# Performance work log

Measured on AMD Instinct MI355X. Metric: run time of the kernel, lower is better.

The kernel has to match this reference:

```python
import jax, jax.numpy as jnp
import numpy as np

H, W = 192, 256
NEAR, FAR = 0.1, 100.0
ALPHA_MAX = 0.99


def setup_inputs() -> dict:
    key = jax.random.key(0)
    k0, k1, k2, k3, k4 = jax.random.split(key, 5)
    N = 512
    # place cloud in front of camera (identity view matrix looks down +z here)
    positions = jax.random.normal(k0, (N, 3), dtype=jnp.float32) + jnp.array([0.0, 0.0, 4.0], jnp.float32)
    scales = jax.random.uniform(k1, (N, 3), dtype=jnp.float32) * 0.2 + 0.02
    rotations = jax.random.normal(k2, (N, 4), dtype=jnp.float32)
    opacities = jax.random.normal(k3, (N, 1), dtype=jnp.float32)
    colors = jax.random.uniform(k4, (N, 3), dtype=jnp.float32)
    view_matrix = jnp.eye(4, dtype=jnp.float32)
    background = jnp.ones(3, dtype=jnp.float32)
    return dict(positions=positions, scales=scales, rotations=rotations,
                opacities=opacities, colors=colors, view_matrix=view_matrix,
                background=background, fov_x=60)


def _quat_to_rot(q):
    q = q / jnp.linalg.norm(q, axis=-1, keepdims=True)
    w, x, y, z = q[:, 0], q[:, 1], q[:, 2], q[:, 3]
    R = jnp.stack([
        1 - 2 * (y * y + z * z), 2 * (x * y - w * z), 2 * (x * z + w * y),
        2 * (x * y + w * z), 1 - 2 * (x * x + z * z), 2 * (y * z - w * x),
        2 * (x * z - w * y), 2 * (y * z + w * x), 1 - 2 * (x * x + y * y)
    ], axis=-1).reshape(-1, 3, 3)
    return R


def reference(positions, scales, rotations, opacities, colors, view_matrix, background, fov_x):
    # --- 3D covariance: R diag(s^2) R^T ---
    R = _quat_to_rot(rotations)                               # (N,3,3)
    cov3d = jnp.einsum('nij,nj,nkj->nik', R, scales ** 2, R)  # (N,3,3)

    # --- projection to screen space ---
    fx = W / (2.0 * np.tan(np.deg2rad(float(fov_x)) / 2.0))
    Wr = view_matrix[:3, :3]
    t = view_matrix[:3, 3]
    cam = positions @ Wr.T + t[None, :]                       # (N,3)
    depths = cam[:, 2]
    zs = jnp.maximum(depths, NEAR)
    X, Y = cam[:, 0], cam[:, 1]
    mx = fx * X / zs + W / 2.0
    my = H / 2.0 - fx * Y / zs
    zero = jnp.zeros_like(zs)
    # Jacobian of perspective projection (N,2,3)
    J = jnp.stack([
        jnp.stack([fx / zs, zero, -fx * X / zs ** 2], axis=-1),
        jnp.stack([zero, fx / zs, -fx * Y / zs ** 2], axis=-1),
    ], axis=1)
    T = jnp.einsum('nij,jk->nik', J, Wr)                      # (N,2,3)
    cov2d = jnp.einsum('nij,njk,nlk->nil', T, cov3d, T)       # (N,2,2)
    cov2d = 0.5 * (cov2d + jnp.swapaxes(cov2d, 1, 2))

    a, b, c = cov2d[:, 0, 0], cov2d[:, 0, 1], cov2d[:, 1, 1]
    mean_e = 0.5 * (a + c)
    disc = jnp.sqrt(jnp.maximum(0.25 * (a - c) ** 2 + b ** 2, 0.0))
    min_eig = mean_e - disc
    eps = jnp.where(min_eig <= 0, jnp.abs(min_eig) + 1e-6, 0.0)
    a = a + eps
    c = c + eps
    max_eig = mean_e + eps + disc
    radii = jnp.ceil(3.0 * jnp.sqrt(jnp.maximum(max_eig, 1e-6)))

    # --- visibility + back-to-front (descending depth) order ---
    visible = (depths > NEAR) & (depths < FAR) & (radii > 0)
    order = jnp.argsort(jnp.where(visible, -depths, jnp.inf))
    a_s, b_s, c_s = a[order], b[order], c[order]
    mx_s, my_s = mx[order], my[order]
    op_s = jax.nn.sigmoid(opacities[order, 0])
    col_s = colors[order]
    vis_s = visible[order].astype(jnp.float32)

    # conic (inverse of 2x2 covariance)
    det = jnp.maximum(a_s * c_s - b_s * b_s, 1e-12)
    ca, cb, cc = c_s / det, -b_s / det, a_s / det

    xs = jnp.arange(W, dtype=jnp.float32)
    ys = jnp.arange(H, dtype=jnp.float32)
    dx = xs[None, None, :] - mx_s[:, None, None]              # (N,H,W)
    dy = ys[None, :, None] - my_s[:, None, None]              # (N,H,W)
    q = (ca[:, None, None] * dx * dx + 2.0 * cb[:, None, None] * dx * dy
         + cc[:, None, None] * dy * dy)
    G = jnp.exp(-0.5 * jnp.maximum(q, 0.0))                   # (N,H,W)
    alpha = jnp.clip(op_s[:, None, None] * G, 0.0, ALPHA_MAX) * vis_s[:, None, None]

    # exclusive cumulative transmittance T_i = prod_{j<i} (1 - alpha_j)
    Tc = jnp.cumprod(1.0 - alpha, axis=0)                     # (N,H,W)
    T_excl = jnp.concatenate([jnp.ones((1, H, W), alpha.dtype), Tc[:-1]], axis=0)
    image = jnp.einsum('nhw,nc->hwc', alpha * T_excl, col_s)  # (H,W,3)
    image = image + Tc[-1][..., None] * background[None, None, :]
    return image


if __name__ == '__main__':
    out = reference(**setup_inputs())
    print(out.shape, out.dtype)
```

## Files before the change

### kernel.cpp

```cpp
#include <hip/hip_runtime.h>
#include <math.h>

#define NG    512
#define IMG_W 256
#define IMG_H 192

#define NEAR_P    0.1f
#define FAR_P     100.0f
#define ALPHA_MAX 0.99f

#define PIX     64
#define CHUNKS  4
#define TPB     256

#define CULL_K  4.0f


__global__ __launch_bounds__(TPB) void gs_fused(
    const float* __restrict__ pos,
    const float* __restrict__ scl,
    const float* __restrict__ rot,
    const float* __restrict__ opa,
    const float* __restrict__ col,
    const float* __restrict__ vm,
    const int*   __restrict__ fov,
    const float* __restrict__ bg,
    float* __restrict__ out)
{
    __shared__ float4 s_cr0[NG];
    __shared__ float4 s_rec1[NG];
    __shared__ float  s_bcol[NG];
    __shared__ __align__(16) unsigned long long s_ku[NG + 2];
    __shared__ unsigned short s_list[NG];
    __shared__ int    s_wtot[4], s_woff[4], s_M, s_Mf;
    __shared__ float4 s_part[CHUNKS][PIX];
    __shared__ float  s_out[PIX*3];

    const int tid  = threadIdx.x;
    const int lane = tid & 63;
    const int wv   = tid >> 6;
    const int b    = blockIdx.x;
    const float yf  = (float)(b >> 2);
    const float x0f = (float)((b & 3) * PIX);

    const float fx = (float)IMG_W /
        (2.0f * __tanf((float)fov[0] * (float)(M_PI / 180.0) * 0.5f));

    const float W00 = vm[0],  W01 = vm[1],  W02 = vm[2],  t0 = vm[3];
    const float W10 = vm[4],  W11 = vm[5],  W12 = vm[6],  t1 = vm[7];
    const float W20 = vm[8],  W21 = vm[9],  W22 = vm[10], t2 = vm[11];

    #pragma unroll
    for (int gg = 0; gg < 2; ++gg) {
        const int g = tid + gg * TPB;
        float px = pos[g*3+0], py = pos[g*3+1], pz = pos[g*3+2];
        float X = W00*px + W01*py + W02*pz + t0;
        float Y = W10*px + W11*py + W12*pz + t1;
        float Z = W20*px + W21*py + W22*pz + t2;

        float zs = fmaxf(Z, NEAR_P);
        float rz = __fdividef(1.0f, zs);
        float fxrz = fx * rz;

        float mx = fxrz * X + (float)IMG_W * 0.5f;
        float my = (float)IMG_H * 0.5f - fxrz * Y;

        float s0 = scl[g*3+0], s1 = scl[g*3+1], s2 = scl[g*3+2];
        float smax2 = fmaxf(fmaxf(s0*s0, s1*s1), s2*s2);
        float Xr = X * rz, Yr = Y * rz;
        float J2 = fxrz*fxrz * (1.0f + Xr*Xr + Yr*Yr);
        float rb = CULL_K * sqrtf(smax2 * J2 + 1e-5f);

        bool visible = (Z > NEAR_P) && (Z < FAR_P);
        s_cr0[g] = make_float4(mx,
                               visible ? my : 1e30f,
                               visible ? rb : 0.0f,
                               visible ? -Z : INFINITY);
    }
    __syncthreads();

    const int g0 = 2*tid, g1 = g0 + 1;
    float4 cr0 = s_cr0[g0];
    float4 cr1 = s_cr0[g1];
    bool p0 = (fabsf(cr0.y - yf) <= cr0.z) &
              (cr0.x >= x0f - cr0.z) & (cr0.x <= x0f + 63.0f + cr0.z);
    bool p1 = (fabsf(cr1.y - yf) <= cr1.z) &
              (cr1.x >= x0f - cr1.z) & (cr1.x <= x0f + 63.0f + cr1.z);

    unsigned long long m0 = __ballot(p0);
    unsigned long long m1 = __ballot(p1);
    unsigned long long lt = (1ull << lane) - 1ull;

    if (lane == 0) s_wtot[wv] = __popcll(m0) + __popcll(m1);
    __syncthreads();
    if (tid == 0) {
        int acc = 0;
        for (int i = 0; i < 4; ++i) { s_woff[i] = acc; acc += s_wtot[i]; }
        s_M = acc;
        s_Mf = 0;
        s_ku[acc]     = ~0ull;
        s_ku[acc + 1] = ~0ull;
    }
    __syncthreads();
    int basep = s_woff[wv] + __popcll(m0 & lt) + __popcll(m1 & lt);
    if (p0) {
        unsigned u = __float_as_uint(cr0.w);
        unsigned mm = (u & 0x80000000u) ? ~u : (u | 0x80000000u);
        s_list[basep] = (unsigned short)g0;
        s_ku[basep] = (((unsigned long long)mm) << 16) | (unsigned)g0;
    }
    if (p1) {
        int p = basep + (p0 ? 1 : 0);
        unsigned u = __float_as_uint(cr1.w);
        unsigned mm = (u & 0x80000000u) ? ~u : (u | 0x80000000u);
        s_list[p] = (unsigned short)g1;
        s_ku[p] = (((unsigned long long)mm) << 16) | (unsigned)g1;
    }
    __syncthreads();

    const int M = s_M;

    bool   qpA[2]   = {false, false};
    float4 rec0A[2], rec1A[2];
    float  bcolA[2] = {0.0f, 0.0f};
    unsigned long long ktA[2] = {0, 0};

    #pragma unroll
    for (int half = 0; half < 2; ++half) {
        if (half == 1 && M <= TPB) continue;
        const int t = half * TPB + tid;
        bool qp = false;
        if (t < M) {
            const int g = s_list[t];
            ktA[half] = s_ku[t];

            float4 q4 = ((const float4*)rot)[g];
            float qw = q4.x, qx = q4.y, qy = q4.z, qz = q4.w;
            float rn = __frsqrt_rn(qw*qw + qx*qx + qy*qy + qz*qz);
            qw *= rn; qx *= rn; qy *= rn; qz *= rn;
            float R00 = 1.f - 2.f*(qy*qy + qz*qz);
            float R01 = 2.f*(qx*qy - qw*qz);
            float R02 = 2.f*(qx*qz + qw*qy);
            float R10 = 2.f*(qx*qy + qw*qz);
            float R11 = 1.f - 2.f*(qx*qx + qz*qz);
            float R12 = 2.f*(qy*qz - qw*qx);
            float R20 = 2.f*(qx*qz - qw*qy);
            float R21 = 2.f*(qy*qz + qw*qx);
            float R22 = 1.f - 2.f*(qx*qx + qy*qy);

            float s0 = scl[g*3+0], s1 = scl[g*3+1], s2 = scl[g*3+2];
            float q0 = s0*s0, q1 = s1*s1, q2 = s2*s2;
            float C00 = R00*R00*q0 + R01*R01*q1 + R02*R02*q2;
            float C01 = R00*R10*q0 + R01*R11*q1 + R02*R12*q2;
            float C02 = R00*R20*q0 + R01*R21*q1 + R02*R22*q2;
            float C11 = R10*R10*q0 + R11*R11*q1 + R12*R12*q2;
            float C12 = R10*R20*q0 + R11*R21*q1 + R12*R22*q2;
            float C22 = R20*R20*q0 + R21*R21*q1 + R22*R22*q2;

            float px = pos[g*3+0], py = pos[g*3+1], pz = pos[g*3+2];
            float X = W00*px + W01*py + W02*pz + t0;
            float Y = W10*px + W11*py + W12*pz + t1;
            float Z = W20*px + W21*py + W22*pz + t2;

            float zs = fmaxf(Z, NEAR_P);
            float rz = __fdividef(1.0f, zs);
            float fxrz = fx * rz;

            float mx = fxrz * X + (float)IMG_W * 0.5f;
            float my = (float)IMG_H * 0.5f - fxrz * Y;

            float j02 = -fxrz * X * rz;
            float j12 = -fxrz * Y * rz;
            float T00 = fxrz*W00 + j02*W20;
            float T01 = fxrz*W01 + j02*W21;
            float T02 = fxrz*W02 + j02*W22;
            float T10 = fxrz*W10 + j12*W20;
            float T11 = fxrz*W11 + j12*W21;
            float T12 = fxrz*W12 + j12*W22;

            float u0 = C00*T00 + C01*T01 + C02*T02;
            float u1 = C01*T00 + C11*T01 + C12*T02;
            float u2 = C02*T00 + C12*T01 + C22*T02;
            float v0 = C00*T10 + C01*T11 + C02*T12;
            float v1 = C01*T10 + C11*T11 + C12*T12;
            float v2 = C02*T10 + C12*T11 + C22*T12;
            float a    = T00*u0 + T01*u1 + T02*u2;
            float bcov = 0.5f * ((T00*v0 + T01*v1 + T02*v2) + (T10*u0 + T11*u1 + T12*u2));
            float c    = T10*v0 + T11*v1 + T12*v2;

            float mean_e = 0.5f * (a + c);
            float disc = sqrtf(fmaxf(0.25f*(a - c)*(a - c) + bcov*bcov, 0.0f));
            float min_eig = mean_e - disc;
            float eps = (min_eig <= 0.0f) ? (fabsf(min_eig) + 1e-6f) : 0.0f;
            a += eps; c += eps;

            float det  = fmaxf(a*c - bcov*bcov, 1e-12f);
            float rdet = __fdividef(1.0f, det);
            float ca = c * rdet, cbv = -bcov * rdet, cc = a * rdet;
            float op = __fdividef(1.0f, 1.0f + __expf(-opa[g]));

            float ex = CULL_K * sqrtf(fmaxf(a, 0.0f));
            float ey = CULL_K * sqrtf(fmaxf(c, 0.0f));
            qp = (fabsf(my - yf) <= ey) &
                 (mx >= x0f - ex) & (mx <= x0f + 63.0f + ex);

            rec0A[half] = make_float4(-0.5f*ca, -cbv, -0.5f*cc, mx);
            rec1A[half] = make_float4(my, op, col[g*3+0], col[g*3+1]);
            bcolA[half] = col[g*3+2];

            if (!qp) s_ku[t] = ~0ull;
        }
        unsigned long long mq = __ballot(qp);
        if (lane == 0) atomicAdd(&s_Mf, __popcll(mq));
        qpA[half] = qp;
    }
    __syncthreads();

    #pragma unroll
    for (int half = 0; half < 2; ++half) {
        if (half == 1 && M <= TPB) continue;
        const int t = half * TPB + tid;
        if (t < M && qpA[half]) {
            const unsigned long long kt = ktA[half];
            const ulonglong2* ku2 = (const ulonglong2*)s_ku;
            int r = 0;
            const int M2 = (M + 1) >> 1;
            for (int j = 0; j < M2; ++j) {
                ulonglong2 kv = ku2[j];
                r += (int)(kv.x < kt);
                r += (int)(kv.y < kt);
            }
            s_cr0[r]  = rec0A[half];
            s_rec1[r] = rec1A[half];
            s_bcol[r] = bcolA[half];
        }
    }
    __syncthreads();

    const int Mf = s_Mf;
    const int qn = (Mf + CHUNKS - 1) / CHUNKS;
    const int lpix  = tid & 63;
    const int chunk = tid >> 6;
    int start = chunk * qn; if (start > Mf) start = Mf;
    int end   = start + qn; if (end > Mf) end = Mf;

    const float fxp = x0f + (float)lpix;

    float Tr = 1.0f, ar = 0.0f, ag = 0.0f, abv = 0.0f;
    for (int i = start; i < end; ++i) {
        float4 r0 = s_cr0[i];
        float4 r1 = s_rec1[i];
        float  bc = s_bcol[i];
        float dx = fxp - r0.w;
        float dy = yf  - r1.x;
        float qv = (r0.x*dx)*dx + (r0.y*dx)*dy + (r0.z*dy)*dy;
        float G = __expf(fminf(qv, 0.0f));
        float alpha = fminf(r1.y * G, ALPHA_MAX);
        float wgt = alpha * Tr;
        ar  += wgt * r1.z;
        ag  += wgt * r1.w;
        abv += wgt * bc;
        Tr  *= (1.0f - alpha);
    }
    s_part[chunk][lpix] = make_float4(ar, ag, abv, Tr);
    __syncthreads();

    if (chunk == 0) {
        float4 c0 = s_part[0][lpix], c1 = s_part[1][lpix];
        float4 c2 = s_part[2][lpix], c3 = s_part[3][lpix];
        float T0 = c0.w, T01 = T0*c1.w, T012 = T01*c2.w, Tall = T012*c3.w;
        float r  = c0.x + T0*c1.x + T01*c2.x + T012*c3.x;
        float gc = c0.y + T0*c1.y + T01*c2.y + T012*c3.y;
        float bb = c0.z + T0*c1.z + T01*c2.z + T012*c3.z;
        s_out[3*lpix+0] = r  + Tall * bg[0];
        s_out[3*lpix+1] = gc + Tall * bg[1];
        s_out[3*lpix+2] = bb + Tall * bg[2];
    }
    __syncthreads();
    if (tid < PIX*3)
        out[b * (PIX*3) + tid] = s_out[tid];
}

extern "C" void kernel_launch(void* const* d_in, const int* in_sizes, int n_in,
                              void* d_out, int out_size, void* d_ws, size_t ws_size,
                              hipStream_t stream) {
    const float* pos = (const float*)d_in[0];
    const float* scl = (const float*)d_in[1];
    const float* rot = (const float*)d_in[2];
    const float* opa = (const float*)d_in[3];
    const float* col = (const float*)d_in[4];
    const float* vm  = (const float*)d_in[5];
    const float* bgp = (const float*)d_in[6];
    const int*   fov = (const int*)d_in[7];

    float* out = (float*)d_out;

    gs_fused<<<(IMG_H * IMG_W) / PIX, TPB, 0, stream>>>(
        pos, scl, rot, opa, col, vm, fov, bgp, out);
}
```

Before: 14.83 us.

## Stage inputs in LDS, fuse culling pass, use 32-bit sort keys

Positions and scales are loaded once per block into shared memory with coalesced float4 loads, and both the cull pass and the per-Gaussian setup read them from there. The coarse cull predicate and depth key are now computed in registers, which removes a shared-memory round trip and a barrier. The rank sort compares 32-bit depth keys, four per LDS read, with an index tie-break in place of the 64-bit key that packed the index. A union lets the staged input buffers share space with the later record and partial-sum arrays to save LDS, and it also drops a redundant clamp before sqrt. The risk is that depth ties now resolve by compacted-list position rather than Gaussian index, and that the union reuse depends on the barriers placed between its phases.

```diff
diff --git a/kernel.cpp b/kernel.cpp
--- a/kernel.cpp
+++ b/kernel.cpp
@@ -15,6 +15,11 @@
 
 #define CULL_K  4.0f
 
+
+union SB {
+    struct { float pos[NG*3]; float scl[NG*3]; } st;
+    struct { float4 rec1[NG]; float4 part[CHUNKS][PIX]; } cp;
+};
 
 __global__ __launch_bounds__(TPB) void gs_fused(
     const float* __restrict__ pos,
@@ -27,13 +32,12 @@
     const float* __restrict__ bg,
     float* __restrict__ out)
 {
-    __shared__ float4 s_cr0[NG];
-    __shared__ float4 s_rec1[NG];
+    __shared__ SB sb;
+    __shared__ float4 s_rec0[NG];
     __shared__ float  s_bcol[NG];
-    __shared__ __align__(16) unsigned long long s_ku[NG + 2];
+    __shared__ __align__(16) unsigned s_ku[NG + 4];
     __shared__ unsigned short s_list[NG];
-    __shared__ int    s_wtot[4], s_woff[4], s_M, s_Mf;
-    __shared__ float4 s_part[CHUNKS][PIX];
+    __shared__ int    s_wtot[8], s_Mf;
     __shared__ float  s_out[PIX*3];
 
     const int tid  = threadIdx.x;
@@ -50,10 +54,26 @@
     const float W10 = vm[4],  W11 = vm[5],  W12 = vm[6],  t1 = vm[7];
     const float W20 = vm[8],  W21 = vm[9],  W22 = vm[10], t2 = vm[11];
 
+    {
+        const float4* p4 = (const float4*)pos;
+        const float4* s4 = (const float4*)scl;
+        float4* dp = (float4*)sb.st.pos;
+        float4* ds = (float4*)sb.st.scl;
+        if (tid < (NG*3)/4) dp[tid] = p4[tid];
+        int j = tid - (NG*3)/4;
+        if (j >= 0) ds[j] = s4[j];
+        int i2 = tid + TPB;
+        if (i2 < (NG*3)/4) dp[i2] = p4[i2];
+        for (int i = tid; i < (NG*3)/4; i += TPB) ds[i] = s4[i];
+    }
+    __syncthreads();
+
+    bool  pr[2];
+    unsigned key32[2];
     #pragma unroll
     for (int gg = 0; gg < 2; ++gg) {
         const int g = tid + gg * TPB;
-        float px = pos[g*3+0], py = pos[g*3+1], pz = pos[g*3+2];
+        float px = sb.st.pos[g*3+0], py = sb.st.pos[g*3+1], pz = sb.st.pos[g*3+2];
         float X = W00*px + W01*py + W02*pz + t0;
         float Y = W10*px + W11*py + W12*pz + t1;
         float Z = W20*px + W21*py + W22*pz + t2;
@@ -65,65 +85,59 @@
         float mx = fxrz * X + (float)IMG_W * 0.5f;
         float my = (float)IMG_H * 0.5f - fxrz * Y;
 
-        float s0 = scl[g*3+0], s1 = scl[g*3+1], s2 = scl[g*3+2];
+        float s0 = sb.st.scl[g*3+0], s1 = sb.st.scl[g*3+1], s2 = sb.st.scl[g*3+2];
         float smax2 = fmaxf(fmaxf(s0*s0, s1*s1), s2*s2);
         float Xr = X * rz, Yr = Y * rz;
         float J2 = fxrz*fxrz * (1.0f + Xr*Xr + Yr*Yr);
         float rb = CULL_K * sqrtf(smax2 * J2 + 1e-5f);
 
         bool visible = (Z > NEAR_P) && (Z < FAR_P);
-        s_cr0[g] = make_float4(mx,
-                               visible ? my : 1e30f,
-                               visible ? rb : 0.0f,
-                               visible ? -Z : INFINITY);
-    }
-    __syncthreads();
-
-    const int g0 = 2*tid, g1 = g0 + 1;
-    float4 cr0 = s_cr0[g0];
-    float4 cr1 = s_cr0[g1];
-    bool p0 = (fabsf(cr0.y - yf) <= cr0.z) &
-              (cr0.x >= x0f - cr0.z) & (cr0.x <= x0f + 63.0f + cr0.z);
-    bool p1 = (fabsf(cr1.y - yf) <= cr1.z) &
-              (cr1.x >= x0f - cr1.z) & (cr1.x <= x0f + 63.0f + cr1.z);
-
-    unsigned long long m0 = __ballot(p0);
-    unsigned long long m1 = __ballot(p1);
+        pr[gg] = visible &
+                 (fabsf(my - yf) <= rb) &
+                 (mx >= x0f - rb) & (mx <= x0f + 63.0f + rb);
+
+        unsigned u = __float_as_uint(-Z);
+        key32[gg] = (u & 0x80000000u) ? ~u : (u | 0x80000000u);
+    }
+
+    unsigned long long m0 = __ballot(pr[0]);
+    unsigned long long m1 = __ballot(pr[1]);
     unsigned long long lt = (1ull << lane) - 1ull;
-
-    if (lane == 0) s_wtot[wv] = __popcll(m0) + __popcll(m1);
-    __syncthreads();
-    if (tid == 0) {
-        int acc = 0;
-        for (int i = 0; i < 4; ++i) { s_woff[i] = acc; acc += s_wtot[i]; }
-        s_M = acc;
-        s_Mf = 0;
-        s_ku[acc]     = ~0ull;
-        s_ku[acc + 1] = ~0ull;
-    }
-    __syncthreads();
-    int basep = s_woff[wv] + __popcll(m0 & lt) + __popcll(m1 & lt);
-    if (p0) {
-        unsigned u = __float_as_uint(cr0.w);
-        unsigned mm = (u & 0x80000000u) ? ~u : (u | 0x80000000u);
-        s_list[basep] = (unsigned short)g0;
-        s_ku[basep] = (((unsigned long long)mm) << 16) | (unsigned)g0;
-    }
-    if (p1) {
-        int p = basep + (p0 ? 1 : 0);
-        unsigned u = __float_as_uint(cr1.w);
-        unsigned mm = (u & 0x80000000u) ? ~u : (u | 0x80000000u);
-        s_list[p] = (unsigned short)g1;
-        s_ku[p] = (((unsigned long long)mm) << 16) | (unsigned)g1;
-    }
-    __syncthreads();
-
-    const int M = s_M;
+    if (lane == 0) {
+        s_wtot[wv]     = __popcll(m0);
+        s_wtot[4 + wv] = __popcll(m1);
+        if (tid == 0) s_Mf = 0;
+    }
+    __syncthreads();
+
+    int w8[8];
+    #pragma unroll
+    for (int i = 0; i < 8; ++i) w8[i] = s_wtot[i];
+    int pref0 = 0, pref1 = 0, M = 0;
+    #pragma unroll
+    for (int i = 0; i < 8; ++i) {
+        if (i < wv)     pref0 += w8[i];
+        if (i < 4 + wv) pref1 += w8[i];
+        M += w8[i];
+    }
+
+    if (pr[0]) {
+        int p = pref0 + __popcll(m0 & lt);
+        s_list[p] = (unsigned short)tid;
+        s_ku[p]   = key32[0];
+    }
+    if (pr[1]) {
+        int p = pref1 + __popcll(m1 & lt);
+        s_list[p] = (unsigned short)(tid + TPB);
+        s_ku[p]   = key32[1];
+    }
+    if (tid < 4) s_ku[M + tid] = 0xFFFFFFFFu;
+    __syncthreads();
 
     bool   qpA[2]   = {false, false};
     float4 rec0A[2], rec1A[2];
     float  bcolA[2] = {0.0f, 0.0f};
-    unsigned long long ktA[2] = {0, 0};
+    unsigned ktA[2] = {0, 0};
 
     #pragma unroll
     for (int half = 0; half < 2; ++half) {
@@ -148,7 +162,7 @@
             float R21 = 2.f*(qy*qz + qw*qx);
             float R22 = 1.f - 2.f*(qx*qx + qy*qy);
 
-            float s0 = scl[g*3+0], s1 = scl[g*3+1], s2 = scl[g*3+2];
+            float s0 = sb.st.scl[g*3+0], s1 = sb.st.scl[g*3+1], s2 = sb.st.scl[g*3+2];
             float q0 = s0*s0, q1 = s1*s1, q2 = s2*s2;
             float C00 = R00*R00*q0 + R01*R01*q1 + R02*R02*q2;
             float C01 = R00*R10*q0 + R01*R11*q1 + R02*R12*q2;
@@ -157,7 +171,7 @@
             float C12 = R10*R20*q0 + R11*R21*q1 + R12*R22*q2;
             float C22 = R20*R20*q0 + R21*R21*q1 + R22*R22*q2;
 
-            float px = pos[g*3+0], py = pos[g*3+1], pz = pos[g*3+2];
+            float px = sb.st.pos[g*3+0], py = sb.st.pos[g*3+1], pz = sb.st.pos[g*3+2];
             float X = W00*px + W01*py + W02*pz + t0;
             float Y = W10*px + W11*py + W12*pz + t1;
             float Z = W20*px + W21*py + W22*pz + t2;
@@ -199,8 +213,8 @@
             float ca = c * rdet, cbv = -bcov * rdet, cc = a * rdet;
             float op = __fdividef(1.0f, 1.0f + __expf(-opa[g]));
 
-            float ex = CULL_K * sqrtf(fmaxf(a, 0.0f));
-            float ey = CULL_K * sqrtf(fmaxf(c, 0.0f));
+            float ex = CULL_K * sqrtf(a);
+            float ey = CULL_K * sqrtf(c);
             qp = (fabsf(my - yf) <= ey) &
                  (mx >= x0f - ex) & (mx <= x0f + 63.0f + ex);
 
@@ -208,7 +222,7 @@
             rec1A[half] = make_float4(my, op, col[g*3+0], col[g*3+1]);
             bcolA[half] = col[g*3+2];
 
-            if (!qp) s_ku[t] = ~0ull;
+            if (!qp) s_ku[t] = 0xFFFFFFFFu;
         }
         unsigned long long mq = __ballot(qp);
         if (lane == 0) atomicAdd(&s_Mf, __popcll(mq));
@@ -221,18 +235,21 @@
         if (half == 1 && M <= TPB) continue;
         const int t = half * TPB + tid;
         if (t < M && qpA[half]) {
-            const unsigned long long kt = ktA[half];
-            const ulonglong2* ku2 = (const ulonglong2*)s_ku;
+            const unsigned kt = ktA[half];
+            const uint4* ku4 = (const uint4*)s_ku;
             int r = 0;
-            const int M2 = (M + 1) >> 1;
-            for (int j = 0; j < M2; ++j) {
-                ulonglong2 kv = ku2[j];
-                r += (int)(kv.x < kt);
-                r += (int)(kv.y < kt);
+            const int M4 = (M + 3) >> 2;
+            for (int j4 = 0; j4 < M4; ++j4) {
+                uint4 kv = ku4[j4];
+                int j = 4*j4;
+                r += (int)((kv.x < kt) | ((kv.x == kt) & (j     < t)));
+                r += (int)((kv.y < kt) | ((kv.y == kt) & (j + 1 < t)));
+                r += (int)((kv.z < kt) | ((kv.z == kt) & (j + 2 < t)));
+                r += (int)((kv.w < kt) | ((kv.w == kt) & (j + 3 < t)));
             }
-            s_cr0[r]  = rec0A[half];
-            s_rec1[r] = rec1A[half];
-            s_bcol[r] = bcolA[half];
+            s_rec0[r]       = rec0A[half];
+            sb.cp.rec1[r]   = rec1A[half];
+            s_bcol[r]       = bcolA[half];
         }
     }
     __syncthreads();
@@ -248,8 +265,8 @@
 
     float Tr = 1.0f, ar = 0.0f, ag = 0.0f, abv = 0.0f;
     for (int i = start; i < end; ++i) {
-        float4 r0 = s_cr0[i];
-        float4 r1 = s_rec1[i];
+        float4 r0 = s_rec0[i];
+        float4 r1 = sb.cp.rec1[i];
         float  bc = s_bcol[i];
         float dx = fxp - r0.w;
         float dy = yf  - r1.x;
@@ -262,12 +279,12 @@
         abv += wgt * bc;
         Tr  *= (1.0f - alpha);
     }
-    s_part[chunk][lpix] = make_float4(ar, ag, abv, Tr);
+    sb.cp.part[chunk][lpix] = make_float4(ar, ag, abv, Tr);
     __syncthreads();
 
     if (chunk == 0) {
-        float4 c0 = s_part[0][lpix], c1 = s_part[1][lpix];
-        float4 c2 = s_part[2][lpix], c3 = s_part[3][lpix];
+        float4 c0 = sb.cp.part[0][lpix], c1 = sb.cp.part[1][lpix];
+        float4 c2 = sb.cp.part[2][lpix], c3 = sb.cp.part[3][lpix];
         float T0 = c0.w, T01 = T0*c1.w, T012 = T01*c2.w, Tall = T012*c3.w;
         float r  = c0.x + T0*c1.x + T01*c2.x + T012*c3.x;
         float gc = c0.y + T0*c1.y + T01*c2.y + T012*c3.y;
```

Measured after the change: 17.90 us. 20.6% more time.
